# Kernel optimization log

Hardware: AMD Instinct MI355X
Metric: run time of the kernel (lower is better)

## Reference

```python
import jax, jax.numpy as jnp
import numpy as np

LAST_Q = 64      # queries used for dynamic pattern estimation (MInference default)
V_TOPK = 1024    # number of vertical (column) indices kept
S_TOPK = 2048    # number of slash (diagonal) offsets kept
FORCE_V = 30     # first columns always kept
FORCE_S = 100    # most-recent diagonals always kept


def setup_inputs() -> dict:
    key = jax.random.key(0)
    kq, kk, kv = jax.random.split(key, 3)
    B, H, S, D = 1, 8, 4096, 128
    q = jax.random.normal(kq, (B, H, S, D), dtype=jnp.float32)
    k = jax.random.normal(kk, (B, H, S, D), dtype=jnp.float32)
    v = jax.random.normal(kv, (B, H, S, D), dtype=jnp.float32)
    return {"q": q, "k": k, "v": v}


def _vertical_slash_attention(q, k, v):
    B, H, S, D = q.shape
    scale = 1.0 / np.sqrt(D).astype(np.float32)

    # ---- pattern estimation on the last LAST_Q queries ----
    qk = jnp.einsum('bhqd,bhkd->bhqk', q[:, :, -LAST_Q:], k) * scale  # [B,H,LQ,S]
    qpos = S - LAST_Q + jnp.arange(LAST_Q)                            # query positions
    causal_last = qpos[:, None] >= jnp.arange(S)[None, :]             # [LQ,S]
    qk = jnp.where(causal_last, qk, jnp.finfo(qk.dtype).min)
    qk = jax.nn.softmax(qk, axis=-1)

    # vertical (column) scores
    vertical = qk.sum(axis=2)                                         # [B,H,S]
    vertical = vertical.at[..., :FORCE_V].set(jnp.inf)
    v_idx = jax.lax.top_k(vertical, V_TOPK)[1]                        # column ids [B,H,V_TOPK]

    # slash (diagonal) scores, indexed by distance o = i - j in [0, S)
    dist = qpos[:, None] - jnp.arange(S)[None, :]                     # [LQ,S]
    dist_c = jnp.clip(dist, 0, S - 1)
    slash = jnp.zeros((B, H, S), qk.dtype).at[:, :, dist_c].add(
        jnp.where(dist >= 0, qk, 0.0))                                # [B,H,S]
    slash = slash.at[..., :FORCE_S].set(jnp.inf)
    s_off = jax.lax.top_k(slash, S_TOPK)[1]                           # diagonal offsets [B,H,S_TOPK]

    # ---- build vertical-slash sparsity mask ----
    ar = jnp.arange(S)
    v_mask = (v_idx[..., :, None] == ar).any(axis=-2)                 # [B,H,S] column allowed
    s_mask = (s_off[..., :, None] == ar).any(axis=-2)                 # [B,H,S] offset allowed

    dmat = ar[:, None] - ar[None, :]                                  # [S,S] query-key distance
    causal = dmat >= 0
    allowed = causal & (v_mask[:, :, None, :] | s_mask[:, :, jnp.clip(dmat, 0, S - 1)])

    # ---- sparse (mask-equivalent) attention ----
    scores = jnp.einsum('bhqd,bhkd->bhqk', q, k) * scale              # [B,H,S,S]
    scores = jnp.where(allowed, scores, jnp.finfo(scores.dtype).min)
    probs = jax.nn.softmax(scores, axis=-1)
    return jnp.einsum('bhqk,bhkd->bhqd', probs, v)


def reference(q, k, v):
    return _vertical_slash_attention(q, k, v)
```

## Files before the change

kernel.cpp:

```cpp
#include <hip/hip_runtime.h>
#include <hip/hip_bf16.h>
#include <math.h>

#define S_LEN 4096
#define DHEAD 128
#define NHEAD 8
#define LASTQ 64
#define V_TOPK 1024
#define S_TOPK 2048
#define FORCE_V 30
#define FORCE_S 100

#define SCALE 0.08838834764831845f
#define NEGBIG -3.0e38f

#define NJOBS 111

typedef __attribute__((ext_vector_type(8))) short short8;
typedef __attribute__((ext_vector_type(4))) float floatx4;
typedef unsigned long long u64;

__device__ __forceinline__ unsigned short f2bf(float f) {
    unsigned u = __float_as_uint(f);
    unsigned r = (u + 0x7fffu + ((u >> 16) & 1u)) >> 16;
    return (unsigned short)r;
}
__device__ __forceinline__ float bf2f(unsigned short s) {
    unsigned u = ((unsigned)s) << 16;
    return __uint_as_float(u);
}

__device__ const short jobQ[NJOBS] = {
    0,1,2,3,4, 5,5, 6,6, 7,7, 8,8, 9,9, 10,10,
    11,11,11, 12,12,12, 13,13,13, 14,14,14, 15,15,15,
    16,16,16,16, 17,17,17,17, 18,18,18,18, 19,19,19,19, 20,20,20,20, 21,21,21,21,
    22,22,22,22,22, 23,23,23,23,23, 24,24,24,24,24, 25,25,25,25,25, 26,26,26,26,26,
    27,27,27,27,27,27, 28,28,28,28,28,28, 29,29,29,29,29,29, 30,30,30,30,30,30,
    31,31,31,31,31,31};
__device__ const short jobK0[NJOBS] = {
    0,0,0,0,0, 0,6, 0,7, 0,8, 0,9, 0,10, 0,11,
    0,8,16, 0,9,18, 0,10,19, 0,10,20, 0,11,22,
    0,9,18,26, 0,9,18,27, 0,10,20,29, 0,10,20,30, 0,11,22,32, 0,11,22,33,
    0,10,19,28,37, 0,10,20,30,39, 0,10,20,30,40, 0,11,22,32,42, 0,11,22,33,44,
    0,10,20,29,38,47, 0,10,20,30,40,49, 0,10,20,30,40,50, 0,11,22,32,42,52,
    0,11,22,33,44,54};
__device__ const short jobK1[NJOBS] = {
    2,4,6,8,10, 6,12, 7,14, 8,16, 9,18, 10,20, 11,22,
    8,16,24, 9,18,26, 10,19,28, 10,20,30, 11,22,32,
    9,18,26,34, 9,18,27,36, 10,20,29,38, 10,20,30,40, 11,22,32,42, 11,22,33,44,
    10,19,28,37,46, 10,20,30,39,48, 10,20,30,40,50, 11,22,32,42,52, 11,22,33,44,54,
    10,20,29,38,47,56, 10,20,30,40,49,58, 10,20,30,40,50,60, 11,22,32,42,52,62,
    11,22,33,44,54,64};
__device__ const short pBase[32] = {0,1,2,3,4,5,7,9,11,13,15,17,20,23,26,29,
                                    32,36,40,44,48,52,56,61,66,71,76,81,87,93,99,105};
__device__ const short pCnt[32]  = {1,1,1,1,1,2,2,2,2,2,2,3,3,3,3,3,
                                    4,4,4,4,4,4,5,5,5,5,5,6,6,6,6,6};

__global__ __launch_bounds__(256) void prep(const float* __restrict__ k,
                                            const float* __restrict__ v,
                                            unsigned short* __restrict__ kbf,
                                            unsigned short* __restrict__ vtbf) {
    int b = blockIdx.x, t = threadIdx.x;
    if (b < 512) {
        const float4* src = (const float4*)k;
        int base = b * 2048;
#pragma unroll
        for (int i = 0; i < 8; ++i) {
            int idx = base + i * 256 + t;
            float4 val = src[idx];
            ushort4 o;
            o.x = f2bf(val.x); o.y = f2bf(val.y); o.z = f2bf(val.z); o.w = f2bf(val.w);
            ((ushort4*)kbf)[idx] = o;
        }
    } else {
        int bx = b - 512;
        int h  = bx >> 7;
        int rem = bx & 127;
        int d0 = (rem >> 6) * 64;
        int k0 = (rem & 63) * 64;
        __shared__ __align__(16) unsigned short T[64][72];
#pragma unroll
        for (int it = 0; it < 4; ++it) {
            int idx = t + it * 256;
            int r = idx >> 4, c4 = idx & 15;
            float4 val = *(const float4*)(v + ((size_t)(h * S_LEN) + k0 + r) * DHEAD + d0 + c4 * 4);
            T[c4 * 4 + 0][r] = f2bf(val.x);
            T[c4 * 4 + 1][r] = f2bf(val.y);
            T[c4 * 4 + 2][r] = f2bf(val.z);
            T[c4 * 4 + 3][r] = f2bf(val.w);
        }
        __syncthreads();
#pragma unroll
        for (int it = 0; it < 2; ++it) {
            int idx = t + it * 256;
            int r = idx >> 3, c8 = idx & 7;
            *(uint4*)(vtbf + ((size_t)h * DHEAD + d0 + r) * S_LEN + k0 + c8 * 8) = *(uint4*)&T[r][c8 * 8];
        }
    }
}

__global__ __launch_bounds__(256) void score_qk(const float* __restrict__ q,
                                                const float* __restrict__ k,
                                                float* __restrict__ scores) {
    int h  = blockIdx.x >> 6;
    int kt = blockIdx.x & 63;
    int t  = threadIdx.x;
    int jl = t >> 2, part = t & 3;
    int j  = kt * 64 + jl;

    __shared__ float4 Qs[64 * 32];
    const float4* qbase = (const float4*)(q + ((size_t)h * S_LEN + (S_LEN - LASTQ)) * DHEAD);
    for (int idx = t; idx < 64 * 32; idx += 256) Qs[idx] = qbase[idx];
    __syncthreads();

    float4 kr[8];
    const float4* kp = (const float4*)(k + ((size_t)h * S_LEN + j) * DHEAD) + part * 8;
#pragma unroll
    for (int c = 0; c < 8; ++c) kr[c] = kp[c];

    float* sp = scores + (size_t)h * LASTQ * S_LEN + j;
#pragma unroll 4
    for (int qi = 0; qi < LASTQ; ++qi) {
        const float4* qp4 = Qs + qi * 32 + part * 8;
        float dot = 0.f;
#pragma unroll
        for (int c = 0; c < 8; ++c) {
            float4 a = qp4[c], b = kr[c];
            dot += a.x * b.x + a.y * b.y + a.z * b.z + a.w * b.w;
        }
        dot += __shfl_xor(dot, 1, 64);
        dot += __shfl_xor(dot, 2, 64);
        if (part == 0) {
            int qpos = S_LEN - LASTQ + qi;
            sp[(size_t)qi * S_LEN] = (j <= qpos) ? dot * SCALE : NEGBIG;
        }
    }
}

__global__ __launch_bounds__(256) void row_stats(const float* __restrict__ scores,
                                                 float* __restrict__ m_out,
                                                 float* __restrict__ inv_out) {
    int row  = blockIdx.x * 4 + (threadIdx.x >> 6);
    int lane = threadIdx.x & 63;
    const float4* rp = (const float4*)(scores + (size_t)row * S_LEN);
    float mx = NEGBIG;
    for (int i = lane; i < S_LEN / 4; i += 64) {
        float4 s4 = rp[i];
        mx = fmaxf(mx, fmaxf(fmaxf(s4.x, s4.y), fmaxf(s4.z, s4.w)));
    }
#pragma unroll
    for (int d = 32; d >= 1; d >>= 1) mx = fmaxf(mx, __shfl_xor(mx, d, 64));
    float su = 0.f;
    for (int i = lane; i < S_LEN / 4; i += 64) {
        float4 s4 = rp[i];
        su += __expf(s4.x - mx) + __expf(s4.y - mx) + __expf(s4.z - mx) + __expf(s4.w - mx);
    }
#pragma unroll
    for (int d = 32; d >= 1; d >>= 1) su += __shfl_xor(su, d, 64);
    if (lane == 0) { m_out[row] = mx; inv_out[row] = 1.0f / su; }
}

__global__ __launch_bounds__(1024) void pattern_finish(const float* __restrict__ scores,
                                                       const float* __restrict__ m_all,
                                                       const float* __restrict__ inv_all,
                                                       unsigned* __restrict__ col_mask,
                                                       unsigned* __restrict__ diag_mask) {
    int h   = blockIdx.x >> 1;
    int sel = blockIdx.x & 1;
    int t = threadIdx.x;
    int kwant  = sel ? S_TOPK : V_TOPK;
    int forced = sel ? FORCE_S : FORCE_V;
    unsigned* dst = sel ? (diag_mask + h * 128) : (col_mask + h * 128);

    __shared__ float sm[LASTQ], sv[LASTQ];
    __shared__ unsigned keys[S_LEN];
    __shared__ int hist[256];
    __shared__ int sh_digit, sh_want;

    if (t < LASTQ) { sm[t] = m_all[h * LASTQ + t]; sv[t] = inv_all[h * LASTQ + t]; }
    __syncthreads();

    const float* S0 = scores + (size_t)h * LASTQ * S_LEN;
#pragma unroll
    for (int rep = 0; rep < 4; ++rep) {
        int j = rep * 1024 + t;
        float acc = 0.f;
        if (sel == 0) {
            for (int r = 0; r < LASTQ; ++r)
                acc += __expf(S0[(size_t)r * S_LEN + j] - sm[r]) * sv[r];
        } else {
            for (int r = 0; r < LASTQ; ++r) {
                int idx = (S_LEN - LASTQ) + r - j;
                if (idx >= 0)
                    acc += __expf(S0[(size_t)r * S_LEN + idx] - sm[r]) * sv[r];
            }
        }
        float f = (j < forced) ? __builtin_inff() : acc;
        unsigned u = __float_as_uint(f);
        u = (u & 0x80000000u) ? ~u : (u | 0x80000000u);
        keys[j] = u;
    }
    __syncthreads();

    unsigned prefix = 0;
    int want = kwant;
    for (int shift = 24; shift >= 0; shift -= 8) {
        if (t < 256) hist[t] = 0;
        __syncthreads();
        for (int j = t; j < S_LEN; j += 1024) {
            unsigned key = keys[j];
            bool match = (shift == 24) || (((key ^ prefix) >> (shift + 8)) == 0);
            if (match) atomicAdd(&hist[(key >> shift) & 255u], 1);
        }
        __syncthreads();
        if (t == 0) {
            int cum = 0, d = 255;
            for (; d >= 0; --d) {
                cum += hist[d];
                if (cum >= want) break;
            }
            sh_digit = d;
            sh_want  = want - (cum - hist[d]);
        }
        __syncthreads();
        prefix |= ((unsigned)sh_digit) << shift;
        want = sh_want;
        __syncthreads();
    }
    if (t < 128) {
        unsigned bits = 0;
        for (int b = 0; b < 32; ++b)
            if (keys[t * 32 + b] >= prefix) bits |= (1u << b);
        dst[t] = bits;
    }
}

#define KS_STRIDE 136
#define VT_STRIDE 72
#define PS_STRIDE 72

__global__ __launch_bounds__(256, 2) void sparse_attn_mfma(
        const float* __restrict__ q,
        const unsigned short* __restrict__ kbf,
        const unsigned short* __restrict__ vtbf,
        const unsigned* __restrict__ col_mask,
        const unsigned* __restrict__ diag_mask,
        unsigned short* __restrict__ pO, float* __restrict__ pm, float* __restrict__ pl) {
    int b = blockIdx.x;
    int h = b & 7;
    int job = b >> 3;
    int Q  = jobQ[job];
    int k0 = jobK0[job];
    int k1 = jobK1[job];
    int i0 = Q * 128;
    int t    = threadIdx.x;
    int wave = t >> 6;
    int lane = t & 63;
    int ln16 = lane & 15;
    int quad = lane >> 4;

    __shared__ __align__(16) unsigned short Ks[64 * KS_STRIDE];
    __shared__ __align__(16) unsigned short Vt[128 * VT_STRIDE];
    __shared__ __align__(16) unsigned short Ps[8 * 16 * PS_STRIDE];
    __shared__ u64 allowed[128];
    __shared__ unsigned dmLDS[130];

    if (t < 130) dmLDS[t] = (t < 128) ? diag_mask[h * 128 + t] : 0u;

    short8 qf[2][4];
#pragma unroll
    for (int s = 0; s < 2; ++s) {
        int qrow = i0 + wave * 32 + s * 16 + ln16;
        const float* qp = q + ((size_t)h * S_LEN + qrow) * DHEAD;
#pragma unroll
        for (int ds = 0; ds < 4; ++ds) {
            int base = ds * 32 + quad * 8;
            float4 a = *(const float4*)(qp + base);
            float4 c = *(const float4*)(qp + base + 4);
            union { unsigned short u[8]; short8 v; } tmp;
            tmp.u[0] = f2bf(a.x * SCALE); tmp.u[1] = f2bf(a.y * SCALE);
            tmp.u[2] = f2bf(a.z * SCALE); tmp.u[3] = f2bf(a.w * SCALE);
            tmp.u[4] = f2bf(c.x * SCALE); tmp.u[5] = f2bf(c.y * SCALE);
            tmp.u[6] = f2bf(c.z * SCALE); tmp.u[7] = f2bf(c.w * SCALE);
            qf[s][ds] = tmp.v;
        }
    }

    floatx4 o4[2][8];
#pragma unroll
    for (int s = 0; s < 2; ++s)
#pragma unroll
        for (int n = 0; n < 8; ++n) o4[s][n] = (floatx4){0.f, 0.f, 0.f, 0.f};
    float m_run[2][4] = {{NEGBIG, NEGBIG, NEGBIG, NEGBIG}, {NEGBIG, NEGBIG, NEGBIG, NEGBIG}};
    float l_run[2][4] = {{0.f, 0.f, 0.f, 0.f}, {0.f, 0.f, 0.f, 0.f}};

    unsigned short* psw[2];
    psw[0] = Ps + (wave * 2 + 0) * 16 * PS_STRIDE;
    psw[1] = Ps + (wave * 2 + 1) * 16 * PS_STRIDE;

    for (int jt = k0; jt < k1; ++jt) {
        int j0 = jt * 64;
        __syncthreads();

#pragma unroll
        for (int it = 0; it < 4; ++it) {
            int idx = t + it * 256;
            int r = idx >> 4, c8 = idx & 15;
            *(uint4*)&Ks[r * KS_STRIDE + c8 * 8] =
                *(const uint4*)(kbf + ((size_t)(h * S_LEN) + j0 + r) * DHEAD + c8 * 8);
        }
#pragma unroll
        for (int it = 0; it < 4; ++it) {
            int idx = t + it * 256;
            int r = idx >> 3, c8 = idx & 7;
            *(uint4*)&Vt[r * VT_STRIDE + c8 * 8] =
                *(const uint4*)(vtbf + ((size_t)h * DHEAD + r) * S_LEN + j0 + c8 * 8);
        }
        if (t < 128) {
            int i = i0 + t;
            int off0 = i - j0;
            u64 a = 0;
            if (off0 >= 0) {
                u64 causal = (off0 >= 63) ? ~0ull : ((1ull << (off0 + 1)) - 1ull);
                u64 cwv = ((u64)col_mask[h * 128 + (j0 >> 5) + 1] << 32) |
                          (u64)col_mask[h * 128 + (j0 >> 5)];
                int sb = off0 - 63;
                u64 V;
                if (sb >= 0) {
                    int w = sb >> 5, sh = sb & 31;
                    u64 lo = ((u64)dmLDS[w + 1] << 32) | (u64)dmLDS[w];
                    u64 hi = (u64)dmLDS[w + 2];
                    V = (lo >> sh) | (sh ? (hi << (64 - sh)) : 0ull);
                } else {
                    u64 w0 = ((u64)dmLDS[1] << 32) | (u64)dmLDS[0];
                    V = w0 << (-sb);
                }
                a = (cwv | __brevll(V)) & causal;
            }
            allowed[t] = a;
        }
        __syncthreads();

        floatx4 sa[2][4];
#pragma unroll
        for (int s = 0; s < 2; ++s)
#pragma unroll
            for (int c = 0; c < 4; ++c) sa[s][c] = (floatx4){0.f, 0.f, 0.f, 0.f};
#pragma unroll
        for (int c = 0; c < 4; ++c) {
            const unsigned short* kbase = Ks + (c * 16 + ln16) * KS_STRIDE + quad * 8;
#pragma unroll
            for (int ds = 0; ds < 4; ++ds) {
                short8 kf = *(const short8*)(kbase + ds * 32);
                sa[0][c] = __builtin_amdgcn_mfma_f32_16x16x32_bf16(qf[0][ds], kf, sa[0][c], 0, 0, 0);
                sa[1][c] = __builtin_amdgcn_mfma_f32_16x16x32_bf16(qf[1][ds], kf, sa[1][c], 0, 0, 0);
            }
        }

#pragma unroll
        for (int s = 0; s < 2; ++s) {
            u64 Arow[4];
#pragma unroll
            for (int r = 0; r < 4; ++r)
                Arow[r] = allowed[wave * 32 + s * 16 + quad * 4 + r];
            float sc[4][4];
#pragma unroll
            for (int c = 0; c < 4; ++c)
#pragma unroll
                for (int r = 0; r < 4; ++r) {
                    bool ok = (Arow[r] >> (c * 16 + ln16)) & 1ull;
                    sc[c][r] = ok ? sa[s][c][r] : -__builtin_inff();
                }
            float mnew[4], alpha[4];
#pragma unroll
            for (int r = 0; r < 4; ++r) {
                float mx = fmaxf(fmaxf(sc[0][r], sc[1][r]), fmaxf(sc[2][r], sc[3][r]));
#pragma unroll
                for (int d = 8; d >= 1; d >>= 1) mx = fmaxf(mx, __shfl_xor(mx, d, 64));
                mnew[r] = fmaxf(m_run[s][r], mx);
                alpha[r] = __expf(m_run[s][r] - mnew[r]);
                m_run[s][r] = mnew[r];
            }
#pragma unroll
            for (int r = 0; r < 4; ++r) {
                float su = 0.f;
                float pvr[4];
#pragma unroll
                for (int c = 0; c < 4; ++c) {
                    float p = __expf(sc[c][r] - mnew[r]);
                    pvr[c] = p;
                    su += p;
                }
#pragma unroll
                for (int c = 0; c < 4; ++c)
                    psw[s][(quad * 4 + r) * PS_STRIDE + c * 16 + ln16] = f2bf(pvr[c]);
#pragma unroll
                for (int d = 8; d >= 1; d >>= 1) su += __shfl_xor(su, d, 64);
                l_run[s][r] = l_run[s][r] * alpha[r] + su;
            }
#pragma unroll
            for (int n = 0; n < 8; ++n)
#pragma unroll
                for (int r = 0; r < 4; ++r) o4[s][n][r] *= alpha[r];
        }
        asm volatile("" ::: "memory");

        short8 pf[2][2];
#pragma unroll
        for (int s = 0; s < 2; ++s) {
            pf[s][0] = *(const short8*)&psw[s][ln16 * PS_STRIDE + quad * 8];
            pf[s][1] = *(const short8*)&psw[s][ln16 * PS_STRIDE + 32 + quad * 8];
        }

#pragma unroll
        for (int n = 0; n < 8; ++n) {
            const unsigned short* vbase = Vt + (n * 16 + ln16) * VT_STRIDE + quad * 8;
            short8 vf0 = *(const short8*)(vbase);
            short8 vf1 = *(const short8*)(vbase + 32);
            o4[0][n] = __builtin_amdgcn_mfma_f32_16x16x32_bf16(pf[0][0], vf0, o4[0][n], 0, 0, 0);
            o4[0][n] = __builtin_amdgcn_mfma_f32_16x16x32_bf16(pf[0][1], vf1, o4[0][n], 0, 0, 0);
            o4[1][n] = __builtin_amdgcn_mfma_f32_16x16x32_bf16(pf[1][0], vf0, o4[1][n], 0, 0, 0);
            o4[1][n] = __builtin_amdgcn_mfma_f32_16x16x32_bf16(pf[1][1], vf1, o4[1][n], 0, 0, 0);
        }
    }

    int pidx = h * NJOBS + job;
    unsigned short* pOp = pO + (size_t)pidx * (128 * DHEAD);
#pragma unroll
    for (int s = 0; s < 2; ++s)
#pragma unroll
        for (int r = 0; r < 4; ++r) {
            int row = wave * 32 + s * 16 + quad * 4 + r;
            if (ln16 == 0) {
                pm[pidx * 128 + row] = m_run[s][r];
                pl[pidx * 128 + row] = l_run[s][r];
            }
#pragma unroll
            for (int n = 0; n < 8; ++n)
                pOp[row * DHEAD + n * 16 + ln16] = f2bf(o4[s][n][r]);
        }
}

__global__ __launch_bounds__(256) void merge_out(const unsigned short* __restrict__ pO,
                                                 const float* __restrict__ pm,
                                                 const float* __restrict__ pl,
                                                 float* __restrict__ out) {
    int b = blockIdx.x;
    int h = b >> 5, Q = b & 31;
    int t = threadIdx.x;
    int row = t >> 1, half = t & 1;
    int p0 = h * NJOBS + pBase[Q];
    int cnt = pCnt[Q];

    float mp[6], lp[6];
    float ms = NEGBIG;
    for (int p = 0; p < cnt; ++p) {
        mp[p] = pm[(p0 + p) * 128 + row];
        lp[p] = pl[(p0 + p) * 128 + row];
        ms = fmaxf(ms, mp[p]);
    }
    float denom = 0.f, w[6];
    for (int p = 0; p < cnt; ++p) {
        w[p] = __expf(mp[p] - ms);
        denom += w[p] * lp[p];
    }
    float invl = 1.0f / denom;

    float acc[64];
#pragma unroll
    for (int i = 0; i < 64; ++i) acc[i] = 0.f;
    for (int p = 0; p < cnt; ++p) {
        const unsigned short* Op = pO + (size_t)(p0 + p) * (128 * DHEAD) + row * DHEAD + half * 64;
        float wp = w[p];
#pragma unroll
        for (int g = 0; g < 8; ++g) {
            ushort4 u0 = ((const ushort4*)Op)[g * 2];
            ushort4 u1 = ((const ushort4*)Op)[g * 2 + 1];
            acc[g * 8 + 0] += wp * bf2f(u0.x); acc[g * 8 + 1] += wp * bf2f(u0.y);
            acc[g * 8 + 2] += wp * bf2f(u0.z); acc[g * 8 + 3] += wp * bf2f(u0.w);
            acc[g * 8 + 4] += wp * bf2f(u1.x); acc[g * 8 + 5] += wp * bf2f(u1.y);
            acc[g * 8 + 6] += wp * bf2f(u1.z); acc[g * 8 + 7] += wp * bf2f(u1.w);
        }
    }
    float* op = out + ((size_t)h * S_LEN + Q * 128 + row) * DHEAD + half * 64;
#pragma unroll
    for (int g = 0; g < 16; ++g) {
        float4 c;
        c.x = acc[g * 4 + 0] * invl; c.y = acc[g * 4 + 1] * invl;
        c.z = acc[g * 4 + 2] * invl; c.w = acc[g * 4 + 3] * invl;
        ((float4*)op)[g] = c;
    }
}

extern "C" void kernel_launch(void* const* d_in, const int* in_sizes, int n_in,
                              void* d_out, int out_size, void* d_ws, size_t ws_size,
                              hipStream_t stream) {
    const float* q = (const float*)d_in[0];
    const float* k = (const float*)d_in[1];
    const float* v = (const float*)d_in[2];
    float* out = (float*)d_out;

    unsigned* col_m  = (unsigned*)d_ws;
    unsigned* diag_m = col_m + 1024;
    float* m_all   = (float*)(diag_m + 1024);
    float* inv_all = m_all + 512;
    unsigned short* kbf  = (unsigned short*)(inv_all + 512);
    unsigned short* vtbf = kbf + (size_t)NHEAD * S_LEN * DHEAD;
    float* scores = (float*)(vtbf + (size_t)NHEAD * S_LEN * DHEAD);
    unsigned short* pO = (unsigned short*)(scores + (size_t)NHEAD * LASTQ * S_LEN);
    float* pm = (float*)(pO + (size_t)8 * NJOBS * 128 * DHEAD);
    float* pl = pm + 8 * NJOBS * 128;

    prep<<<1536, 256, 0, stream>>>(k, v, kbf, vtbf);
    score_qk<<<NHEAD * 64, 256, 0, stream>>>(q, k, scores);
    row_stats<<<NHEAD * LASTQ / 4, 256, 0, stream>>>(scores, m_all, inv_all);
    pattern_finish<<<NHEAD * 2, 1024, 0, stream>>>(scores, m_all, inv_all, col_m, diag_m);
    sparse_attn_mfma<<<NHEAD * NJOBS, 256, 0, stream>>>(q, kbf, vtbf, col_m, diag_m, pO, pm, pl);
    merge_out<<<NHEAD * 32, 256, 0, stream>>>(pO, pm, pl, out);
}
```

Measured before the change: 301.5 us.

## Fuse prep and score kernels, prefetch K/V tiles, swizzle LDS, lazy rescale

Merges the bf16 conversion/transpose kernel with the last-query score kernel into one launch with shared LDS. In the sparse attention kernel it register-prefetches the next K/V tile while the current one is processed. It replaces padded LDS strides with XOR swizzling and raises the occupancy hint to 3 blocks. It also adds s_setprio around the MFMA sections and skips the online-softmax rescale when no row max increases. Together these target launch overhead, global-load latency and LDS footprint, at the cost of higher register pressure from the prefetch buffers.

```diff
diff --git a/kernel.cpp b/kernel.cpp
--- a/kernel.cpp
+++ b/kernel.cpp
@@ -56,11 +56,15 @@
 __device__ const short pCnt[32]  = {1,1,1,1,1,2,2,2,2,2,2,3,3,3,3,3,
                                     4,4,4,4,4,4,5,5,5,5,5,6,6,6,6,6};
 
-__global__ __launch_bounds__(256) void prep(const float* __restrict__ k,
-                                            const float* __restrict__ v,
-                                            unsigned short* __restrict__ kbf,
-                                            unsigned short* __restrict__ vtbf) {
+__global__ __launch_bounds__(256) void prep_score(const float* __restrict__ q,
+                                                  const float* __restrict__ k,
+                                                  const float* __restrict__ v,
+                                                  unsigned short* __restrict__ kbf,
+                                                  unsigned short* __restrict__ vtbf,
+                                                  float* __restrict__ scores) {
     int b = blockIdx.x, t = threadIdx.x;
+    __shared__ __align__(16) float4 SH[64 * 32];
+
     if (b < 512) {
         const float4* src = (const float4*)k;
         int base = b * 2048;
@@ -72,13 +76,13 @@
             o.x = f2bf(val.x); o.y = f2bf(val.y); o.z = f2bf(val.z); o.w = f2bf(val.w);
             ((ushort4*)kbf)[idx] = o;
         }
-    } else {
+    } else if (b < 1536) {
         int bx = b - 512;
         int h  = bx >> 7;
         int rem = bx & 127;
         int d0 = (rem >> 6) * 64;
         int k0 = (rem & 63) * 64;
-        __shared__ __align__(16) unsigned short T[64][72];
+        unsigned short (*T)[72] = reinterpret_cast<unsigned short(*)[72]>(SH);
 #pragma unroll
         for (int it = 0; it < 4; ++it) {
             int idx = t + it * 256;
@@ -96,43 +100,39 @@
             int r = idx >> 3, c8 = idx & 7;
             *(uint4*)(vtbf + ((size_t)h * DHEAD + d0 + r) * S_LEN + k0 + c8 * 8) = *(uint4*)&T[r][c8 * 8];
         }
-    }
-}
-
-__global__ __launch_bounds__(256) void score_qk(const float* __restrict__ q,
-                                                const float* __restrict__ k,
-                                                float* __restrict__ scores) {
-    int h  = blockIdx.x >> 6;
-    int kt = blockIdx.x & 63;
-    int t  = threadIdx.x;
-    int jl = t >> 2, part = t & 3;
-    int j  = kt * 64 + jl;
-
-    __shared__ float4 Qs[64 * 32];
-    const float4* qbase = (const float4*)(q + ((size_t)h * S_LEN + (S_LEN - LASTQ)) * DHEAD);
-    for (int idx = t; idx < 64 * 32; idx += 256) Qs[idx] = qbase[idx];
-    __syncthreads();
-
-    float4 kr[8];
-    const float4* kp = (const float4*)(k + ((size_t)h * S_LEN + j) * DHEAD) + part * 8;
-#pragma unroll
-    for (int c = 0; c < 8; ++c) kr[c] = kp[c];
-
-    float* sp = scores + (size_t)h * LASTQ * S_LEN + j;
+    } else {
+        int bx = b - 1536;
+        int h  = bx >> 6;
+        int kt = bx & 63;
+        int jl = t >> 2, part = t & 3;
+        int j  = kt * 64 + jl;
+
+        float4* Qs = (float4*)SH;
+        const float4* qbase = (const float4*)(q + ((size_t)h * S_LEN + (S_LEN - LASTQ)) * DHEAD);
+        for (int idx = t; idx < 64 * 32; idx += 256) Qs[idx] = qbase[idx];
+        __syncthreads();
+
+        float4 kr[8];
+        const float4* kp = (const float4*)(k + ((size_t)h * S_LEN + j) * DHEAD) + part * 8;
+#pragma unroll
+        for (int c = 0; c < 8; ++c) kr[c] = kp[c];
+
+        float* sp = scores + (size_t)h * LASTQ * S_LEN + j;
 #pragma unroll 4
-    for (int qi = 0; qi < LASTQ; ++qi) {
-        const float4* qp4 = Qs + qi * 32 + part * 8;
-        float dot = 0.f;
-#pragma unroll
-        for (int c = 0; c < 8; ++c) {
-            float4 a = qp4[c], b = kr[c];
-            dot += a.x * b.x + a.y * b.y + a.z * b.z + a.w * b.w;
-        }
-        dot += __shfl_xor(dot, 1, 64);
-        dot += __shfl_xor(dot, 2, 64);
-        if (part == 0) {
-            int qpos = S_LEN - LASTQ + qi;
-            sp[(size_t)qi * S_LEN] = (j <= qpos) ? dot * SCALE : NEGBIG;
+        for (int qi = 0; qi < LASTQ; ++qi) {
+            const float4* qp4 = Qs + qi * 32 + part * 8;
+            float dot = 0.f;
+#pragma unroll
+            for (int c = 0; c < 8; ++c) {
+                float4 a = qp4[c], bb = kr[c];
+                dot += a.x * bb.x + a.y * bb.y + a.z * bb.z + a.w * bb.w;
+            }
+            dot += __shfl_xor(dot, 1, 64);
+            dot += __shfl_xor(dot, 2, 64);
+            if (part == 0) {
+                int qpos = S_LEN - LASTQ + qi;
+                sp[(size_t)qi * S_LEN] = (j <= qpos) ? dot * SCALE : NEGBIG;
+            }
         }
     }
 }
@@ -235,11 +235,9 @@
     }
 }
 
-#define KS_STRIDE 136
-#define VT_STRIDE 72
 #define PS_STRIDE 72
 
-__global__ __launch_bounds__(256, 2) void sparse_attn_mfma(
+__global__ __launch_bounds__(256, 3) void sparse_attn_mfma(
         const float* __restrict__ q,
         const unsigned short* __restrict__ kbf,
         const unsigned short* __restrict__ vtbf,
@@ -258,9 +256,10 @@
     int lane = t & 63;
     int ln16 = lane & 15;
     int quad = lane >> 4;
-
-    __shared__ __align__(16) unsigned short Ks[64 * KS_STRIDE];
-    __shared__ __align__(16) unsigned short Vt[128 * VT_STRIDE];
+    int lsw  = ln16 & 7;
+
+    __shared__ __align__(16) unsigned short Ks[64 * 128];
+    __shared__ __align__(16) unsigned short Vt[128 * 64];
     __shared__ __align__(16) unsigned short Ps[8 * 16 * PS_STRIDE];
     __shared__ u64 allowed[128];
     __shared__ unsigned dmLDS[130];
@@ -298,6 +297,25 @@
     psw[0] = Ps + (wave * 2 + 0) * 16 * PS_STRIDE;
     psw[1] = Ps + (wave * 2 + 1) * 16 * PS_STRIDE;
 
+    const unsigned short* kgbase = kbf + (size_t)h * S_LEN * DHEAD;
+    const unsigned short* vgbase = vtbf + (size_t)h * DHEAD * S_LEN;
+
+    uint4 kreg[4], vreg[4];
+    auto load_tile = [&](int j0_) {
+#pragma unroll
+        for (int it = 0; it < 4; ++it) {
+            int idx = t + it * 256;
+            kreg[it] = *(const uint4*)(kgbase + ((size_t)(j0_ + (idx >> 4))) * DHEAD + (idx & 15) * 8);
+        }
+#pragma unroll
+        for (int it = 0; it < 4; ++it) {
+            int idx = t + it * 256;
+            vreg[it] = *(const uint4*)(vgbase + ((size_t)(idx >> 3)) * S_LEN + j0_ + (idx & 7) * 8);
+        }
+    };
+
+    load_tile(k0 * 64);
+
     for (int jt = k0; jt < k1; ++jt) {
         int j0 = jt * 64;
         __syncthreads();
@@ -306,16 +324,16 @@
         for (int it = 0; it < 4; ++it) {
             int idx = t + it * 256;
             int r = idx >> 4, c8 = idx & 15;
-            *(uint4*)&Ks[r * KS_STRIDE + c8 * 8] =
-                *(const uint4*)(kbf + ((size_t)(h * S_LEN) + j0 + r) * DHEAD + c8 * 8);
+            *(uint4*)&Ks[r * 128 + ((c8 ^ (r & 7)) << 3)] = kreg[it];
         }
 #pragma unroll
         for (int it = 0; it < 4; ++it) {
             int idx = t + it * 256;
             int r = idx >> 3, c8 = idx & 7;
-            *(uint4*)&Vt[r * VT_STRIDE + c8 * 8] =
-                *(const uint4*)(vtbf + ((size_t)h * DHEAD + r) * S_LEN + j0 + c8 * 8);
-        }
+            *(uint4*)&Vt[r * 64 + ((c8 ^ (r & 7)) << 3)] = vreg[it];
+        }
+        if (jt + 1 < k1) load_tile(j0 + 64);
+
         if (t < 128) {
             int i = i0 + t;
             int off0 = i - j0;
@@ -346,40 +364,53 @@
         for (int s = 0; s < 2; ++s)
 #pragma unroll
             for (int c = 0; c < 4; ++c) sa[s][c] = (floatx4){0.f, 0.f, 0.f, 0.f};
+        __builtin_amdgcn_s_setprio(1);
 #pragma unroll
         for (int c = 0; c < 4; ++c) {
-            const unsigned short* kbase = Ks + (c * 16 + ln16) * KS_STRIDE + quad * 8;
+            const unsigned short* kbase = Ks + (c * 16 + ln16) * 128;
 #pragma unroll
             for (int ds = 0; ds < 4; ++ds) {
-                short8 kf = *(const short8*)(kbase + ds * 32);
+                short8 kf = *(const short8*)(kbase + (((ds * 4 + quad) ^ lsw) << 3));
                 sa[0][c] = __builtin_amdgcn_mfma_f32_16x16x32_bf16(qf[0][ds], kf, sa[0][c], 0, 0, 0);
                 sa[1][c] = __builtin_amdgcn_mfma_f32_16x16x32_bf16(qf[1][ds], kf, sa[1][c], 0, 0, 0);
             }
         }
+        __builtin_amdgcn_s_setprio(0);
 
 #pragma unroll
         for (int s = 0; s < 2; ++s) {
-            u64 Arow[4];
+            u64 ash[4];
 #pragma unroll
             for (int r = 0; r < 4; ++r)
-                Arow[r] = allowed[wave * 32 + s * 16 + quad * 4 + r];
+                ash[r] = allowed[wave * 32 + s * 16 + quad * 4 + r] >> ln16;
             float sc[4][4];
 #pragma unroll
             for (int c = 0; c < 4; ++c)
 #pragma unroll
                 for (int r = 0; r < 4; ++r) {
-                    bool ok = (Arow[r] >> (c * 16 + ln16)) & 1ull;
+                    bool ok = (ash[r] >> (c * 16)) & 1ull;
                     sc[c][r] = ok ? sa[s][c][r] : -__builtin_inff();
                 }
-            float mnew[4], alpha[4];
+            float mloc[4];
 #pragma unroll
             for (int r = 0; r < 4; ++r) {
                 float mx = fmaxf(fmaxf(sc[0][r], sc[1][r]), fmaxf(sc[2][r], sc[3][r]));
 #pragma unroll
                 for (int d = 8; d >= 1; d >>= 1) mx = fmaxf(mx, __shfl_xor(mx, d, 64));
-                mnew[r] = fmaxf(m_run[s][r], mx);
-                alpha[r] = __expf(m_run[s][r] - mnew[r]);
-                m_run[s][r] = mnew[r];
+                mloc[r] = mx;
+            }
+            bool nd = (mloc[0] > m_run[s][0]) | (mloc[1] > m_run[s][1]) |
+                      (mloc[2] > m_run[s][2]) | (mloc[3] > m_run[s][3]);
+            if (__any((int)nd)) {
+#pragma unroll
+                for (int r = 0; r < 4; ++r) {
+                    float mn = fmaxf(m_run[s][r], mloc[r]);
+                    float al = __expf(m_run[s][r] - mn);
+                    m_run[s][r] = mn;
+                    l_run[s][r] *= al;
+#pragma unroll
+                    for (int n = 0; n < 8; ++n) o4[s][n][r] *= al;
+                }
             }
 #pragma unroll
             for (int r = 0; r < 4; ++r) {
@@ -387,7 +418,7 @@
                 float pvr[4];
 #pragma unroll
                 for (int c = 0; c < 4; ++c) {
-                    float p = __expf(sc[c][r] - mnew[r]);
+                    float p = __expf(sc[c][r] - m_run[s][r]);
                     pvr[c] = p;
                     su += p;
                 }
@@ -396,12 +427,8 @@
                     psw[s][(quad * 4 + r) * PS_STRIDE + c * 16 + ln16] = f2bf(pvr[c]);
 #pragma unroll
                 for (int d = 8; d >= 1; d >>= 1) su += __shfl_xor(su, d, 64);
-                l_run[s][r] = l_run[s][r] * alpha[r] + su;
-            }
-#pragma unroll
-            for (int n = 0; n < 8; ++n)
-#pragma unroll
-                for (int r = 0; r < 4; ++r) o4[s][n][r] *= alpha[r];
+                l_run[s][r] += su;
+            }
         }
         asm volatile("" ::: "memory");
 
@@ -412,16 +439,18 @@
             pf[s][1] = *(const short8*)&psw[s][ln16 * PS_STRIDE + 32 + quad * 8];
         }
 
+        __builtin_amdgcn_s_setprio(1);
 #pragma unroll
         for (int n = 0; n < 8; ++n) {
-            const unsigned short* vbase = Vt + (n * 16 + ln16) * VT_STRIDE + quad * 8;
-            short8 vf0 = *(const short8*)(vbase);
-            short8 vf1 = *(const short8*)(vbase + 32);
+            const unsigned short* vbase = Vt + (n * 16 + ln16) * 64;
+            short8 vf0 = *(const short8*)(vbase + ((quad ^ lsw) << 3));
+            short8 vf1 = *(const short8*)(vbase + (((quad + 4) ^ lsw) << 3));
             o4[0][n] = __builtin_amdgcn_mfma_f32_16x16x32_bf16(pf[0][0], vf0, o4[0][n], 0, 0, 0);
             o4[0][n] = __builtin_amdgcn_mfma_f32_16x16x32_bf16(pf[0][1], vf1, o4[0][n], 0, 0, 0);
             o4[1][n] = __builtin_amdgcn_mfma_f32_16x16x32_bf16(pf[1][0], vf0, o4[1][n], 0, 0, 0);
             o4[1][n] = __builtin_amdgcn_mfma_f32_16x16x32_bf16(pf[1][1], vf1, o4[1][n], 0, 0, 0);
         }
+        __builtin_amdgcn_s_setprio(0);
     }
 
     int pidx = h * NJOBS + job;
@@ -511,8 +540,7 @@
     float* pm = (float*)(pO + (size_t)8 * NJOBS * 128 * DHEAD);
     float* pl = pm + 8 * NJOBS * 128;
 
-    prep<<<1536, 256, 0, stream>>>(k, v, kbf, vtbf);
-    score_qk<<<NHEAD * 64, 256, 0, stream>>>(q, k, scores);
+    prep_score<<<2048, 256, 0, stream>>>(q, k, v, kbf, vtbf, scores);
     row_stats<<<NHEAD * LASTQ / 4, 256, 0, stream>>>(scores, m_all, inv_all);
     pattern_finish<<<NHEAD * 2, 1024, 0, stream>>>(scores, m_all, inv_all, col_m, diag_m);
     sparse_attn_mfma<<<NHEAD * NJOBS, 256, 0, stream>>>(q, kbf, vtbf, col_m, diag_m, pO, pm, pl);
```

After: 487.6 us. +61.7%, slower.
